# Optimization experiments

Hardware: AMD Instinct MI355X
Metric: run time of the kernel (lower is better)

Reference implementation:

```python
import jax, jax.numpy as jnp
import numpy as np

N_Q = 16
N_K = 16
D_QK = 64
D_V = 64
# torch module default scale=1.0 saturates softmax at feature width 1024;
# we use the conventional sqrt(d) scale for well-conditioned numerics.
SCALE = 32.0  # sqrt(N_Q * D_QK)
DROPOUT_P = 0.0  # dropout is identity at p=0


def setup_inputs() -> dict:
    key = jax.random.key(0)
    kq, kk, kv = jax.random.split(key, 3)
    S = 8192
    return {
        "query": jax.random.normal(kq, (S, N_Q, D_QK), dtype=jnp.float32),
        "key": jax.random.normal(kk, (S, N_K, D_QK), dtype=jnp.float32),
        "value": jax.random.normal(kv, (S, N_K, D_V), dtype=jnp.float32),
    }


def reference(query, key, value):
    # Flatten trailing (head, dim) into one feature axis, as the torch view does.
    q = query.reshape(-1, N_Q * D_QK)            # [S_q, 1024]
    k = key.reshape(-1, N_K * D_QK)              # [S_k, 1024]
    v = value.reshape(-1, N_K * D_V)             # [S_k, 1024]
    scores = jnp.matmul(q, k.T) / SCALE          # [S_q, S_k]
    attn = jax.nn.softmax(scores, axis=-1)       # dropout_p=0 -> identity
    out = jnp.matmul(attn, v)                    # [S_q, 1024]
    return out.reshape(query.shape[:-1] + (-1,))  # [S_q, N_Q, D_V]
```

## Files before the change

### kernel.cpp

```cpp
#include <hip/hip_runtime.h>
#include <hip/hip_bf16.h>


typedef __bf16 bf16x8 __attribute__((ext_vector_type(8)));
typedef float f32x4 __attribute__((ext_vector_type(4)));
typedef const __attribute__((address_space(1))) unsigned int* as1p;
typedef __attribute__((address_space(3))) unsigned int* as3p;
typedef unsigned short u16;

__device__ __forceinline__ u16 f2bf(float x) {
  unsigned u = __float_as_uint(x);
  u += 0x7fffu + ((u >> 16) & 1u);
  return (u16)(u >> 16);
}
__device__ __forceinline__ float bf2f(u16 b) { return __uint_as_float(((unsigned)b) << 16); }
__device__ __forceinline__ unsigned pack2(float lo, float hi) {
  return (unsigned)f2bf(lo) | ((unsigned)f2bf(hi) << 16);
}

#define BARX()   __builtin_amdgcn_s_barrier()
#define WAITL()  asm volatile("s_waitcnt lgkmcnt(0)")
#define WAITV(n) asm volatile("s_waitcnt vmcnt(" #n ")")

__global__ __launch_bounds__(256) void cvt_bf16(const float* __restrict__ in,
                                                unsigned short* __restrict__ out) {
  const size_t i = (size_t)blockIdx.x * 256 + threadIdx.x;
  const float4* p = (const float4*)in + i * 2;
  float4 a = p[0], b = p[1];
  uint4 o;
  o.x = pack2(a.x, a.y);
  o.y = pack2(a.z, a.w);
  o.z = pack2(b.x, b.y);
  o.w = pack2(b.z, b.w);
  ((uint4*)out)[i] = o;
}

__global__ __launch_bounds__(256) void transpose_bf16(const float* __restrict__ V,
                                                      unsigned short* __restrict__ VT) {
  __shared__ float t[64][65];
  const int rb = blockIdx.x * 64;
  const int cb = blockIdx.y * 64;
  const int tid = threadIdx.x;
#pragma unroll
  for (int it = 0; it < 4; ++it) {
    int r = it * 16 + (tid >> 4);
    int c = (tid & 15) * 4;
    float4 x = *(const float4*)(V + (size_t)(rb + r) * 1024 + cb + c);
    t[r][c] = x.x; t[r][c + 1] = x.y; t[r][c + 2] = x.z; t[r][c + 3] = x.w;
  }
  __syncthreads();
  const int j = tid & 63;
  const int c0 = (tid >> 6) * 16;
#pragma unroll
  for (int i = 0; i < 16; ++i) {
    int c = c0 + i;
    VT[(size_t)(cb + c) * 8192 + rb + j] = f2bf(t[j][c]);
  }
}

template <int BM, int OUTMODE, int DEC>
__global__ __launch_bounds__(512, 2) void gemm8d(const u16* __restrict__ A,
                                                 const u16* __restrict__ B,
                                                 void* __restrict__ Cv,
                                                 const float* __restrict__ inv,
                                                 float* __restrict__ partials,
                                                 int K, int ldc, float scale) {
  constexpr int MF = BM / 32;
  constexpr int MH = MF / 2;
  constexpr int ABUF = BM * 128;
  constexpr int BBUF = 32768;
  constexpr int BUFSZ = ABUF + BBUF;
  __shared__ __align__(1024) char smem[2 * BUFSZ];

  const int tid = threadIdx.x;
  const int lane = tid & 63, wave = tid >> 6;
  const int wr = wave >> 2, wc = wave & 3;
  const int lan15 = lane & 15, g = lane >> 4, l7 = lane & 7;

  const int nwg = gridDim.x;
  const int wg = (blockIdx.x & 7) * (nwg >> 3) + (blockIdx.x >> 3);
  int bm0, bn0;
  if constexpr (DEC == 0) {
    const int r = wg & 255;
    bm0 = (r >> 3) * 256;
    bn0 = (((wg >> 8) << 3) | (r & 7)) * 256;
  } else {
    const int chunk = wg >> 5;
    const int within = wg & 31;
    bm0 = (chunk * 8 + (within >> 2)) * BM;
    bn0 = (within & 3) * 256;
  }

  const int sr = tid >> 3;
  const int scb = ((tid & 7) ^ (sr & 7)) * 8;
  const u16* Ags = A + (size_t)(bm0 + sr) * K + scb;
  const u16* Bgs = B + (size_t)(bn0 + sr) * K + scb;

  const int sa0 = ((0 + g) ^ l7) * 16;
  const int sa1 = ((4 + g) ^ l7) * 16;
  const int abase = (wr * (BM / 2) + lan15) * 128;
  const int bbase = ABUF + (wc * 64 + lan15) * 128;

  f32x4 acc[MF][4];
#pragma unroll
  for (int m = 0; m < MF; ++m)
#pragma unroll
    for (int n = 0; n < 4; ++n) acc[m][n] = f32x4{0.f, 0.f, 0.f, 0.f};

  const int nt = K >> 6;
  const int niter = nt >> 1;

  auto IA = [&](int t, int ja, int jb) {
    char* bb = smem + (t & 1) * BUFSZ;
    const size_t ko = (size_t)t * 64;
    __builtin_amdgcn_global_load_lds((as1p)(Ags + (size_t)ja * 64 * K + ko),
                                     (as3p)(bb + ja * 8192 + tid * 16), 16, 0, 0);
    __builtin_amdgcn_global_load_lds((as1p)(Ags + (size_t)jb * 64 * K + ko),
                                     (as3p)(bb + jb * 8192 + tid * 16), 16, 0, 0);
  };
  auto IB = [&](int t, int j0) {
    char* bb = smem + (t & 1) * BUFSZ + ABUF;
    const size_t ko = (size_t)t * 64;
    __builtin_amdgcn_global_load_lds((as1p)(Bgs + (size_t)j0 * 64 * K + ko),
                                     (as3p)(bb + j0 * 8192 + tid * 16), 16, 0, 0);
    __builtin_amdgcn_global_load_lds((as1p)(Bgs + (size_t)(j0 + 1) * 64 * K + ko),
                                     (as3p)(bb + (j0 + 1) * 8192 + tid * 16), 16, 0, 0);
  };
  auto IA_mh0 = [&](int t) { if constexpr (BM == 256) IA(t, 0, 2); };
  auto IA_mh1 = [&](int t) { if constexpr (BM == 256) IA(t, 1, 3); else IA(t, 0, 1); };

  bf16x8 a[MH][2], b[4][2];
  auto DS_A = [&](int bb, int mh) {
#pragma unroll
    for (int m = 0; m < MH; ++m) {
      a[m][0] = *(const bf16x8*)(smem + bb + abase + (mh * MH + m) * 2048 + sa0);
      a[m][1] = *(const bf16x8*)(smem + bb + abase + (mh * MH + m) * 2048 + sa1);
    }
  };
  auto DS_B = [&](int bb, int nh) {
#pragma unroll
    for (int n = 0; n < 2; ++n) {
      b[nh * 2 + n][0] = *(const bf16x8*)(smem + bb + bbase + (nh * 2 + n) * 2048 + sa0);
      b[nh * 2 + n][1] = *(const bf16x8*)(smem + bb + bbase + (nh * 2 + n) * 2048 + sa1);
    }
  };
  auto MMA = [&](int mh, int nh) {
    __builtin_amdgcn_s_setprio(1);
#pragma unroll
    for (int m = 0; m < MH; ++m)
#pragma unroll
      for (int n = 0; n < 2; ++n)
#pragma unroll
        for (int ks = 0; ks < 2; ++ks)
          acc[mh * MH + m][nh * 2 + n] = __builtin_amdgcn_mfma_f32_16x16x32_bf16(
              a[m][ks], b[nh * 2 + n][ks], acc[mh * MH + m][nh * 2 + n], 0, 0, 0);
    __builtin_amdgcn_s_setprio(0);
  };

  if constexpr (BM == 256) {
    IA(0, 0, 2); IB(0, 0); IB(0, 2); IA(0, 1, 3);
    IA(1, 0, 2); IB(1, 0); IB(1, 2);
    WAITV(6);
  } else {
    IB(0, 0); IB(0, 2); IA(0, 0, 1);
    IB(1, 0); IB(1, 2);
    WAITV(4);
  }
  BARX();

  for (int i = 0; i < niter; ++i) {
    const int t0 = 2 * i;
    const bool more = (i + 1 < niter);

    DS_A(0, 0); DS_B(0, 0);
    IA_mh1(t0 + 1);
    BARX(); WAITL(); MMA(0, 0); BARX();

    DS_B(0, 1);
    if (more) IA_mh0(t0 + 2);
    BARX(); WAITL(); MMA(0, 1); BARX();

    DS_A(0, 1);
    if (more) IB(t0 + 2, 0);
    BARX(); WAITL(); MMA(1, 0); BARX();

    if (more) IB(t0 + 2, 2);
    BARX(); MMA(1, 1);
    if (more) { if constexpr (BM == 256) WAITV(6); else WAITV(4); } else { WAITV(0); }
    BARX();

    DS_A(BUFSZ, 0); DS_B(BUFSZ, 0);
    if (more) IA_mh1(t0 + 2);
    BARX(); WAITL(); MMA(0, 0); BARX();

    DS_B(BUFSZ, 1);
    if (more) IA_mh0(t0 + 3);
    BARX(); WAITL(); MMA(0, 1); BARX();

    DS_A(BUFSZ, 1);
    if (more) IB(t0 + 3, 0);
    BARX(); WAITL(); MMA(1, 0); BARX();

    if (more) IB(t0 + 3, 2);
    BARX(); MMA(1, 1);
    if (more) { if constexpr (BM == 256) WAITV(6); else WAITV(4); } else { WAITV(0); }
    BARX();
  }

  const int c0 = bn0 + wc * 64 + lan15;
  if constexpr (OUTMODE == 0) {
    u16* C = (u16*)Cv;
    const int cb4 = (bn0 >> 8) * 4 + wc;
#pragma unroll
    for (int m = 0; m < MF; ++m)
#pragma unroll
      for (int r = 0; r < 4; ++r) {
        const int row = bm0 + wr * (BM / 2) + m * 16 + g * 4 + r;
        float part = 0.f;
#pragma unroll
        for (int n = 0; n < 4; ++n) {
          float v = __expf(acc[m][n][r] * scale);
          C[(size_t)row * ldc + c0 + n * 16] = f2bf(v);
          part += v;
        }
        part += __shfl_xor(part, 1, 64);
        part += __shfl_xor(part, 2, 64);
        part += __shfl_xor(part, 4, 64);
        part += __shfl_xor(part, 8, 64);
        if (lan15 == 0) partials[(size_t)row * 128 + cb4] = part;
      }
  } else {
    float* C = (float*)Cv;
#pragma unroll
    for (int m = 0; m < MF; ++m)
#pragma unroll
      for (int r = 0; r < 4; ++r) {
        const int row = bm0 + wr * (BM / 2) + m * 16 + g * 4 + r;
        const float iv = inv ? inv[row] : 1.0f;
#pragma unroll
        for (int n = 0; n < 4; ++n)
          C[(size_t)row * ldc + c0 + n * 16] = acc[m][n][r] * iv;
      }
  }
}

__global__ __launch_bounds__(256) void rowinv(const float* __restrict__ partials,
                                              float* __restrict__ inv) {
  const int row = blockIdx.x * 256 + threadIdx.x;
  const float4* p = (const float4*)(partials + (size_t)row * 128);
  float s = 0.f;
#pragma unroll
  for (int j = 0; j < 32; ++j) {
    float4 v = p[j];
    s += (v.x + v.y) + (v.z + v.w);
  }
  inv[row] = 1.0f / s;
}

__global__ __launch_bounds__(256) void normalize_inplace(u16* __restrict__ E) {
  __shared__ float red[4];
  u16* row = E + (size_t)blockIdx.x * 8192;
  const int tid = threadIdx.x;
  float f[32];
  float s = 0.f;
#pragma unroll
  for (int c = 0; c < 4; ++c) {
    uint4 v = *((const uint4*)row + c * 256 + tid);
    unsigned u[4] = {v.x, v.y, v.z, v.w};
#pragma unroll
    for (int q = 0; q < 4; ++q) {
      f[c * 8 + q * 2] = bf2f((u16)(u[q] & 0xffffu));
      f[c * 8 + q * 2 + 1] = bf2f((u16)(u[q] >> 16));
      s += f[c * 8 + q * 2] + f[c * 8 + q * 2 + 1];
    }
  }
#pragma unroll
  for (int off = 32; off; off >>= 1) s += __shfl_xor(s, off, 64);
  if ((tid & 63) == 0) red[tid >> 6] = s;
  __syncthreads();
  const float iv = 1.0f / ((red[0] + red[1]) + (red[2] + red[3]));
#pragma unroll
  for (int c = 0; c < 4; ++c) {
    uint4 o;
    o.x = pack2(f[c * 8 + 0] * iv, f[c * 8 + 1] * iv);
    o.y = pack2(f[c * 8 + 2] * iv, f[c * 8 + 3] * iv);
    o.z = pack2(f[c * 8 + 4] * iv, f[c * 8 + 5] * iv);
    o.w = pack2(f[c * 8 + 6] * iv, f[c * 8 + 7] * iv);
    *((uint4*)row + c * 256 + tid) = o;
  }
}

extern "C" void kernel_launch(void* const* d_in, const int* in_sizes, int n_in,
                              void* d_out, int out_size, void* d_ws, size_t ws_size,
                              hipStream_t stream) {
  const float* Q = (const float*)d_in[0];
  const float* K = (const float*)d_in[1];
  const float* V = (const float*)d_in[2];

  char* ws = (char*)d_ws;
  u16* S = (u16*)ws;
  u16* VT = (u16*)(ws + (size_t)134217728);
  float* partials = (float*)(ws + (size_t)134217728 + 16777216);
  float* inv = (float*)(ws + (size_t)134217728 + 16777216 + 4194304);
  const bool haveInv =
      ws_size >= (size_t)134217728 + 16777216 + 4194304 + 32768;

  u16* Qb = (u16*)d_out;
  u16* Kb = Qb + 8388608;

  cvt_bf16<<<4096, 256, 0, stream>>>(Q, Qb);
  cvt_bf16<<<4096, 256, 0, stream>>>(K, Kb);
  transpose_bf16<<<dim3(128, 16), 256, 0, stream>>>(V, VT);

  gemm8d<256, 0, 0><<<1024, 512, 0, stream>>>(
      Qb, Kb, S, nullptr, haveInv ? partials : (float*)(ws + 134217728 + 16777216),
      1024, 8192, 1.0f / 32.0f);

  if (haveInv) {
    rowinv<<<32, 256, 0, stream>>>(partials, inv);
    gemm8d<128, 1, 1><<<256, 512, 0, stream>>>(
        S, VT, d_out, inv, nullptr, 8192, 1024, 1.0f);
  } else {
    normalize_inplace<<<8192, 256, 0, stream>>>(S);
    gemm8d<128, 1, 1><<<256, 512, 0, stream>>>(
        S, VT, d_out, nullptr, nullptr, 8192, 1024, 1.0f);
  }
}
```

Before: 303.0 us.

## Shrink GEMM tiles to 128x128 with four blocks per CU and simpler pipeline

Replaces the 256x256 and 128x256 GEMM tiles with a single 128x128 tile kernel sized for four resident workgroups per CU, with a simplified double-buffered load/MFMA schedule. The grids grow to 4096 and 512 blocks. Row-sum partials for the softmax are now reduced across the four column-waves in LDS before a single write per row, which halves the partials buffer and the rowinv reads. Smaller tiles are meant to raise occupancy and improve load balance. The cost is lower arithmetic intensity per tile and more global traffic for the operands.

After: 319.6 us. 5.5% more time.

```diff
diff --git a/kernel.cpp b/kernel.cpp
--- a/kernel.cpp
+++ b/kernel.cpp
@@ -58,18 +58,15 @@
   }
 }
 
-template <int BM, int OUTMODE, int DEC>
-__global__ __launch_bounds__(512, 2) void gemm8d(const u16* __restrict__ A,
+template <int OUTMODE, int DEC>
+__global__ __launch_bounds__(512, 4) void gemm2b(const u16* __restrict__ A,
                                                  const u16* __restrict__ B,
                                                  void* __restrict__ Cv,
                                                  const float* __restrict__ inv,
                                                  float* __restrict__ partials,
                                                  int K, int ldc, float scale) {
-  constexpr int MF = BM / 32;
-  constexpr int MH = MF / 2;
-  constexpr int ABUF = BM * 128;
-  constexpr int BBUF = 32768;
-  constexpr int BUFSZ = ABUF + BBUF;
+  constexpr int ABUF = 16384;
+  constexpr int BUFSZ = 32768;
   __shared__ __align__(1024) char smem[2 * BUFSZ];
 
   const int tid = threadIdx.x;
@@ -81,14 +78,16 @@
   const int wg = (blockIdx.x & 7) * (nwg >> 3) + (blockIdx.x >> 3);
   int bm0, bn0;
   if constexpr (DEC == 0) {
-    const int r = wg & 255;
-    bm0 = (r >> 3) * 256;
-    bn0 = (((wg >> 8) << 3) | (r & 7)) * 256;
+    const int chunk = wg >> 9;
+    const int r9 = wg & 511;
+    const int sub = r9 >> 6, win = r9 & 63;
+    bm0 = (chunk * 8 + (win >> 3)) * 128;
+    bn0 = (sub * 8 + (win & 7)) * 128;
   } else {
-    const int chunk = wg >> 5;
-    const int within = wg & 31;
-    bm0 = (chunk * 8 + (within >> 2)) * BM;
-    bn0 = (within & 3) * 256;
+    const int chunk = wg >> 6;
+    const int win = wg & 63;
+    bm0 = (chunk * 8 + (win >> 3)) * 128;
+    bn0 = (win & 7) * 128;
   }
 
   const int sr = tid >> 3;
@@ -98,127 +97,109 @@
 
   const int sa0 = ((0 + g) ^ l7) * 16;
   const int sa1 = ((4 + g) ^ l7) * 16;
-  const int abase = (wr * (BM / 2) + lan15) * 128;
-  const int bbase = ABUF + (wc * 64 + lan15) * 128;
-
-  f32x4 acc[MF][4];
-#pragma unroll
-  for (int m = 0; m < MF; ++m)
-#pragma unroll
-    for (int n = 0; n < 4; ++n) acc[m][n] = f32x4{0.f, 0.f, 0.f, 0.f};
+  const int abase = (wr * 64 + lan15) * 128;
+  const int bbase = ABUF + (wc * 32 + lan15) * 128;
+
+  f32x4 acc[4][2];
+#pragma unroll
+  for (int m = 0; m < 4; ++m)
+#pragma unroll
+    for (int n = 0; n < 2; ++n) acc[m][n] = f32x4{0.f, 0.f, 0.f, 0.f};
 
   const int nt = K >> 6;
   const int niter = nt >> 1;
 
-  auto IA = [&](int t, int ja, int jb) {
+  auto IA = [&](int t) {
     char* bb = smem + (t & 1) * BUFSZ;
     const size_t ko = (size_t)t * 64;
-    __builtin_amdgcn_global_load_lds((as1p)(Ags + (size_t)ja * 64 * K + ko),
-                                     (as3p)(bb + ja * 8192 + tid * 16), 16, 0, 0);
-    __builtin_amdgcn_global_load_lds((as1p)(Ags + (size_t)jb * 64 * K + ko),
-                                     (as3p)(bb + jb * 8192 + tid * 16), 16, 0, 0);
-  };
-  auto IB = [&](int t, int j0) {
+    __builtin_amdgcn_global_load_lds((as1p)(Ags + ko),
+                                     (as3p)(bb + tid * 16), 16, 0, 0);
+    __builtin_amdgcn_global_load_lds((as1p)(Ags + (size_t)64 * K + ko),
+                                     (as3p)(bb + 8192 + tid * 16), 16, 0, 0);
+  };
+  auto IB = [&](int t) {
     char* bb = smem + (t & 1) * BUFSZ + ABUF;
     const size_t ko = (size_t)t * 64;
-    __builtin_amdgcn_global_load_lds((as1p)(Bgs + (size_t)j0 * 64 * K + ko),
-                                     (as3p)(bb + j0 * 8192 + tid * 16), 16, 0, 0);
-    __builtin_amdgcn_global_load_lds((as1p)(Bgs + (size_t)(j0 + 1) * 64 * K + ko),
-                                     (as3p)(bb + (j0 + 1) * 8192 + tid * 16), 16, 0, 0);
-  };
-  auto IA_mh0 = [&](int t) { if constexpr (BM == 256) IA(t, 0, 2); };
-  auto IA_mh1 = [&](int t) { if constexpr (BM == 256) IA(t, 1, 3); else IA(t, 0, 1); };
-
-  bf16x8 a[MH][2], b[4][2];
+    __builtin_amdgcn_global_load_lds((as1p)(Bgs + ko),
+                                     (as3p)(bb + tid * 16), 16, 0, 0);
+    __builtin_amdgcn_global_load_lds((as1p)(Bgs + (size_t)64 * K + ko),
+                                     (as3p)(bb + 8192 + tid * 16), 16, 0, 0);
+  };
+
+  bf16x8 a[2][2], b[2][2];
   auto DS_A = [&](int bb, int mh) {
 #pragma unroll
-    for (int m = 0; m < MH; ++m) {
-      a[m][0] = *(const bf16x8*)(smem + bb + abase + (mh * MH + m) * 2048 + sa0);
-      a[m][1] = *(const bf16x8*)(smem + bb + abase + (mh * MH + m) * 2048 + sa1);
+    for (int m = 0; m < 2; ++m) {
+      a[m][0] = *(const bf16x8*)(smem + bb + abase + (mh * 2 + m) * 2048 + sa0);
+      a[m][1] = *(const bf16x8*)(smem + bb + abase + (mh * 2 + m) * 2048 + sa1);
     }
   };
-  auto DS_B = [&](int bb, int nh) {
+  auto DS_B = [&](int bb) {
 #pragma unroll
     for (int n = 0; n < 2; ++n) {
-      b[nh * 2 + n][0] = *(const bf16x8*)(smem + bb + bbase + (nh * 2 + n) * 2048 + sa0);
-      b[nh * 2 + n][1] = *(const bf16x8*)(smem + bb + bbase + (nh * 2 + n) * 2048 + sa1);
+      b[n][0] = *(const bf16x8*)(smem + bb + bbase + n * 2048 + sa0);
+      b[n][1] = *(const bf16x8*)(smem + bb + bbase + n * 2048 + sa1);
     }
   };
-  auto MMA = [&](int mh, int nh) {
+  auto MMA = [&](int mh) {
     __builtin_amdgcn_s_setprio(1);
 #pragma unroll
-    for (int m = 0; m < MH; ++m)
+    for (int m = 0; m < 2; ++m)
 #pragma unroll
       for (int n = 0; n < 2; ++n)
 #pragma unroll
         for (int ks = 0; ks < 2; ++ks)
-          acc[mh * MH + m][nh * 2 + n] = __builtin_amdgcn_mfma_f32_16x16x32_bf16(
-              a[m][ks], b[nh * 2 + n][ks], acc[mh * MH + m][nh * 2 + n], 0, 0, 0);
+          acc[mh * 2 + m][n] = __builtin_amdgcn_mfma_f32_16x16x32_bf16(
+              a[m][ks], b[n][ks], acc[mh * 2 + m][n], 0, 0, 0);
     __builtin_amdgcn_s_setprio(0);
   };
 
-  if constexpr (BM == 256) {
-    IA(0, 0, 2); IB(0, 0); IB(0, 2); IA(0, 1, 3);
-    IA(1, 0, 2); IB(1, 0); IB(1, 2);
-    WAITV(6);
-  } else {
-    IB(0, 0); IB(0, 2); IA(0, 0, 1);
-    IB(1, 0); IB(1, 2);
-    WAITV(4);
-  }
+  IA(0); IB(0); IA(1);
+  WAITV(2);
   BARX();
 
   for (int i = 0; i < niter; ++i) {
     const int t0 = 2 * i;
-    const bool more = (i + 1 < niter);
-
-    DS_A(0, 0); DS_B(0, 0);
-    IA_mh1(t0 + 1);
-    BARX(); WAITL(); MMA(0, 0); BARX();
-
-    DS_B(0, 1);
-    if (more) IA_mh0(t0 + 2);
-    BARX(); WAITL(); MMA(0, 1); BARX();
+    const bool more = (t0 + 2 < nt);
+
+    DS_A(0, 0); DS_B(0);
+    BARX(); WAITL();
+    IB(t0 + 1);
+    MMA(0);
+    BARX();
 
     DS_A(0, 1);
-    if (more) IB(t0 + 2, 0);
-    BARX(); WAITL(); MMA(1, 0); BARX();
-
-    if (more) IB(t0 + 2, 2);
-    BARX(); MMA(1, 1);
-    if (more) { if constexpr (BM == 256) WAITV(6); else WAITV(4); } else { WAITV(0); }
-    BARX();
-
-    DS_A(BUFSZ, 0); DS_B(BUFSZ, 0);
-    if (more) IA_mh1(t0 + 2);
-    BARX(); WAITL(); MMA(0, 0); BARX();
-
-    DS_B(BUFSZ, 1);
-    if (more) IA_mh0(t0 + 3);
-    BARX(); WAITL(); MMA(0, 1); BARX();
+    BARX(); WAITL();
+    if (more) { IA(t0 + 2); MMA(1); WAITV(2); }
+    else      { MMA(1); WAITV(0); }
+    BARX();
+
+    DS_A(BUFSZ, 0); DS_B(BUFSZ);
+    BARX(); WAITL();
+    if (more) IB(t0 + 2);
+    MMA(0);
+    BARX();
 
     DS_A(BUFSZ, 1);
-    if (more) IB(t0 + 3, 0);
-    BARX(); WAITL(); MMA(1, 0); BARX();
-
-    if (more) IB(t0 + 3, 2);
-    BARX(); MMA(1, 1);
-    if (more) { if constexpr (BM == 256) WAITV(6); else WAITV(4); } else { WAITV(0); }
-    BARX();
-  }
-
-  const int c0 = bn0 + wc * 64 + lan15;
+    BARX(); WAITL();
+    if (more) { IA(t0 + 3); MMA(1); WAITV(2); }
+    else      { MMA(1); }
+    BARX();
+  }
+
+  const int c0 = bn0 + wc * 32 + lan15;
   if constexpr (OUTMODE == 0) {
     u16* C = (u16*)Cv;
-    const int cb4 = (bn0 >> 8) * 4 + wc;
-#pragma unroll
-    for (int m = 0; m < MF; ++m)
+    float* red = (float*)smem;
+    float part_rows[4][4];
+#pragma unroll
+    for (int m = 0; m < 4; ++m)
 #pragma unroll
       for (int r = 0; r < 4; ++r) {
-        const int row = bm0 + wr * (BM / 2) + m * 16 + g * 4 + r;
+        const int row = bm0 + wr * 64 + m * 16 + g * 4 + r;
         float part = 0.f;
 #pragma unroll
-        for (int n = 0; n < 4; ++n) {
+        for (int n = 0; n < 2; ++n) {
           float v = __expf(acc[m][n][r] * scale);
           C[(size_t)row * ldc + c0 + n * 16] = f2bf(v);
           part += v;
@@ -227,18 +208,30 @@
         part += __shfl_xor(part, 2, 64);
         part += __shfl_xor(part, 4, 64);
         part += __shfl_xor(part, 8, 64);
-        if (lan15 == 0) partials[(size_t)row * 128 + cb4] = part;
+        part_rows[m][r] = part;
       }
+    BARX();
+#pragma unroll
+    for (int m = 0; m < 4; ++m)
+#pragma unroll
+      for (int r = 0; r < 4; ++r)
+        if (lan15 == 0)
+          red[(wr * 64 + m * 16 + g * 4 + r) * 4 + wc] = part_rows[m][r];
+    __syncthreads();
+    if (tid < 128) {
+      const float4 v = *(const float4*)&red[tid * 4];
+      partials[(size_t)(bm0 + tid) * 64 + (bn0 >> 7)] = (v.x + v.y) + (v.z + v.w);
+    }
   } else {
     float* C = (float*)Cv;
 #pragma unroll
-    for (int m = 0; m < MF; ++m)
+    for (int m = 0; m < 4; ++m)
 #pragma unroll
       for (int r = 0; r < 4; ++r) {
-        const int row = bm0 + wr * (BM / 2) + m * 16 + g * 4 + r;
+        const int row = bm0 + wr * 64 + m * 16 + g * 4 + r;
         const float iv = inv ? inv[row] : 1.0f;
 #pragma unroll
-        for (int n = 0; n < 4; ++n)
+        for (int n = 0; n < 2; ++n)
           C[(size_t)row * ldc + c0 + n * 16] = acc[m][n][r] * iv;
       }
   }
@@ -247,10 +240,10 @@
 __global__ __launch_bounds__(256) void rowinv(const float* __restrict__ partials,
                                               float* __restrict__ inv) {
   const int row = blockIdx.x * 256 + threadIdx.x;
-  const float4* p = (const float4*)(partials + (size_t)row * 128);
+  const float4* p = (const float4*)(partials + (size_t)row * 64);
   float s = 0.f;
 #pragma unroll
-  for (int j = 0; j < 32; ++j) {
+  for (int j = 0; j < 16; ++j) {
     float4 v = p[j];
     s += (v.x + v.y) + (v.z + v.w);
   }
@@ -312,17 +305,17 @@
   cvt_bf16<<<4096, 256, 0, stream>>>(K, Kb);
   transpose_bf16<<<dim3(128, 16), 256, 0, stream>>>(V, VT);
 
-  gemm8d<256, 0, 0><<<1024, 512, 0, stream>>>(
+  gemm2b<0, 0><<<4096, 512, 0, stream>>>(
       Qb, Kb, S, nullptr, haveInv ? partials : (float*)(ws + 134217728 + 16777216),
       1024, 8192, 1.0f / 32.0f);
 
   if (haveInv) {
     rowinv<<<32, 256, 0, stream>>>(partials, inv);
-    gemm8d<128, 1, 1><<<256, 512, 0, stream>>>(
+    gemm2b<1, 1><<<512, 512, 0, stream>>>(
         S, VT, d_out, inv, nullptr, 8192, 1024, 1.0f);
   } else {
     normalize_inplace<<<8192, 256, 0, stream>>>(S);
-    gemm8d<128, 1, 1><<<256, 512, 0, stream>>>(
+    gemm2b<1, 1><<<512, 512, 0, stream>>>(
         S, VT, d_out, nullptr, nullptr, 8192, 1024, 1.0f);
   }
 }
```

## Switch GEMM tiles from 16x16x32 to 32x32x16 bf16 MFMA

Applied to the files above, without the earlier changes.

Replaces the 16x16x32 MFMA fragments with 32x32x16 MFMA. Each wave now holds 32x32 accumulator blocks, and the LDS fragment loads are reorganized into four k-slices with matching swizzle offsets. The epilogue row mapping and the row-sum shuffle reduction are updated for the 32-lane layout. The intent is to cut LDS read traffic per FLOP and raise MFMA throughput per instruction. The cost is a different register and LDS access pattern, which could cause bank conflicts or register pressure.

After: 362.6 us. 1.2x slower.

```diff
diff --git a/kernel.cpp b/kernel.cpp
--- a/kernel.cpp
+++ b/kernel.cpp
@@ -3,7 +3,7 @@
 
 
 typedef __bf16 bf16x8 __attribute__((ext_vector_type(8)));
-typedef float f32x4 __attribute__((ext_vector_type(4)));
+typedef float f32x16 __attribute__((ext_vector_type(16)));
 typedef const __attribute__((address_space(1))) unsigned int* as1p;
 typedef __attribute__((address_space(3))) unsigned int* as3p;
 typedef unsigned short u16;
@@ -59,14 +59,14 @@
 }
 
 template <int BM, int OUTMODE, int DEC>
-__global__ __launch_bounds__(512, 2) void gemm8d(const u16* __restrict__ A,
+__global__ __launch_bounds__(512, 2) void gemm32(const u16* __restrict__ A,
                                                  const u16* __restrict__ B,
                                                  void* __restrict__ Cv,
                                                  const float* __restrict__ inv,
                                                  float* __restrict__ partials,
                                                  int K, int ldc, float scale) {
-  constexpr int MF = BM / 32;
-  constexpr int MH = MF / 2;
+  constexpr int NRB = BM / 64;
+  constexpr int MHT = NRB / 2;
   constexpr int ABUF = BM * 128;
   constexpr int BBUF = 32768;
   constexpr int BUFSZ = ABUF + BBUF;
@@ -75,7 +75,7 @@
   const int tid = threadIdx.x;
   const int lane = tid & 63, wave = tid >> 6;
   const int wr = wave >> 2, wc = wave & 3;
-  const int lan15 = lane & 15, g = lane >> 4, l7 = lane & 7;
+  const int l31 = lane & 31, lg = lane >> 5, l7 = lane & 7;
 
   const int nwg = gridDim.x;
   const int wg = (blockIdx.x & 7) * (nwg >> 3) + (blockIdx.x >> 3);
@@ -96,16 +96,19 @@
   const u16* Ags = A + (size_t)(bm0 + sr) * K + scb;
   const u16* Bgs = B + (size_t)(bn0 + sr) * K + scb;
 
-  const int sa0 = ((0 + g) ^ l7) * 16;
-  const int sa1 = ((4 + g) ^ l7) * 16;
-  const int abase = (wr * (BM / 2) + lan15) * 128;
-  const int bbase = ABUF + (wc * 64 + lan15) * 128;
-
-  f32x4 acc[MF][4];
-#pragma unroll
-  for (int m = 0; m < MF; ++m)
-#pragma unroll
-    for (int n = 0; n < 4; ++n) acc[m][n] = f32x4{0.f, 0.f, 0.f, 0.f};
+  int sk[4];
+#pragma unroll
+  for (int ks = 0; ks < 4; ++ks) sk[ks] = ((ks * 2 + lg) ^ l7) * 16;
+  const int abase = (wr * (BM / 2) + l31) * 128;
+  const int bbase = ABUF + (wc * 64 + l31) * 128;
+
+  f32x16 acc[NRB][2];
+#pragma unroll
+  for (int m = 0; m < NRB; ++m)
+#pragma unroll
+    for (int n = 0; n < 2; ++n)
+#pragma unroll
+      for (int r = 0; r < 16; ++r) acc[m][n][r] = 0.f;
 
   const int nt = K >> 6;
   const int niter = nt >> 1;
@@ -129,31 +132,27 @@
   auto IA_mh0 = [&](int t) { if constexpr (BM == 256) IA(t, 0, 2); };
   auto IA_mh1 = [&](int t) { if constexpr (BM == 256) IA(t, 1, 3); else IA(t, 0, 1); };
 
-  bf16x8 a[MH][2], b[4][2];
+  bf16x8 a[MHT][4], b[2][4];
   auto DS_A = [&](int bb, int mh) {
 #pragma unroll
-    for (int m = 0; m < MH; ++m) {
-      a[m][0] = *(const bf16x8*)(smem + bb + abase + (mh * MH + m) * 2048 + sa0);
-      a[m][1] = *(const bf16x8*)(smem + bb + abase + (mh * MH + m) * 2048 + sa1);
-    }
+    for (int t = 0; t < MHT; ++t)
+#pragma unroll
+      for (int ks = 0; ks < 4; ++ks)
+        a[t][ks] = *(const bf16x8*)(smem + bb + abase + (mh * MHT + t) * 4096 + sk[ks]);
   };
   auto DS_B = [&](int bb, int nh) {
 #pragma unroll
-    for (int n = 0; n < 2; ++n) {
-      b[nh * 2 + n][0] = *(const bf16x8*)(smem + bb + bbase + (nh * 2 + n) * 2048 + sa0);
-      b[nh * 2 + n][1] = *(const bf16x8*)(smem + bb + bbase + (nh * 2 + n) * 2048 + sa1);
-    }
+    for (int ks = 0; ks < 4; ++ks)
+      b[nh][ks] = *(const bf16x8*)(smem + bb + bbase + nh * 4096 + sk[ks]);
   };
   auto MMA = [&](int mh, int nh) {
     __builtin_amdgcn_s_setprio(1);
 #pragma unroll
-    for (int m = 0; m < MH; ++m)
-#pragma unroll
-      for (int n = 0; n < 2; ++n)
-#pragma unroll
-        for (int ks = 0; ks < 2; ++ks)
-          acc[mh * MH + m][nh * 2 + n] = __builtin_amdgcn_mfma_f32_16x16x32_bf16(
-              a[m][ks], b[nh * 2 + n][ks], acc[mh * MH + m][nh * 2 + n], 0, 0, 0);
+    for (int t = 0; t < MHT; ++t)
+#pragma unroll
+      for (int ks = 0; ks < 4; ++ks)
+        acc[mh * MHT + t][nh] = __builtin_amdgcn_mfma_f32_32x32x16_bf16(
+            a[t][ks], b[nh][ks], acc[mh * MHT + t][nh], 0, 0, 0);
     __builtin_amdgcn_s_setprio(0);
   };
 
@@ -207,39 +206,39 @@
     BARX();
   }
 
-  const int c0 = bn0 + wc * 64 + lan15;
+  const int c0 = bn0 + wc * 64 + l31;
   if constexpr (OUTMODE == 0) {
     u16* C = (u16*)Cv;
     const int cb4 = (bn0 >> 8) * 4 + wc;
 #pragma unroll
-    for (int m = 0; m < MF; ++m)
-#pragma unroll
-      for (int r = 0; r < 4; ++r) {
-        const int row = bm0 + wr * (BM / 2) + m * 16 + g * 4 + r;
-        float part = 0.f;
-#pragma unroll
-        for (int n = 0; n < 4; ++n) {
-          float v = __expf(acc[m][n][r] * scale);
-          C[(size_t)row * ldc + c0 + n * 16] = f2bf(v);
-          part += v;
-        }
+    for (int rb = 0; rb < NRB; ++rb)
+#pragma unroll
+      for (int reg = 0; reg < 16; ++reg) {
+        const int row = bm0 + wr * (BM / 2) + rb * 32 +
+                        (reg & 3) + 8 * (reg >> 2) + 4 * lg;
+        const float v0 = __expf(acc[rb][0][reg] * scale);
+        const float v1 = __expf(acc[rb][1][reg] * scale);
+        C[(size_t)row * ldc + c0] = f2bf(v0);
+        C[(size_t)row * ldc + c0 + 32] = f2bf(v1);
+        float part = v0 + v1;
         part += __shfl_xor(part, 1, 64);
         part += __shfl_xor(part, 2, 64);
         part += __shfl_xor(part, 4, 64);
         part += __shfl_xor(part, 8, 64);
-        if (lan15 == 0) partials[(size_t)row * 128 + cb4] = part;
+        part += __shfl_xor(part, 16, 64);
+        if (l31 == 0) partials[(size_t)row * 128 + cb4] = part;
       }
   } else {
     float* C = (float*)Cv;
 #pragma unroll
-    for (int m = 0; m < MF; ++m)
-#pragma unroll
-      for (int r = 0; r < 4; ++r) {
-        const int row = bm0 + wr * (BM / 2) + m * 16 + g * 4 + r;
+    for (int rb = 0; rb < NRB; ++rb)
+#pragma unroll
+      for (int reg = 0; reg < 16; ++reg) {
+        const int row = bm0 + wr * (BM / 2) + rb * 32 +
+                        (reg & 3) + 8 * (reg >> 2) + 4 * lg;
         const float iv = inv ? inv[row] : 1.0f;
-#pragma unroll
-        for (int n = 0; n < 4; ++n)
-          C[(size_t)row * ldc + c0 + n * 16] = acc[m][n][r] * iv;
+        C[(size_t)row * ldc + c0] = acc[rb][0][reg] * iv;
+        C[(size_t)row * ldc + c0 + 32] = acc[rb][1][reg] * iv;
       }
   }
 }
@@ -312,17 +311,17 @@
   cvt_bf16<<<4096, 256, 0, stream>>>(K, Kb);
   transpose_bf16<<<dim3(128, 16), 256, 0, stream>>>(V, VT);
 
-  gemm8d<256, 0, 0><<<1024, 512, 0, stream>>>(
+  gemm32<256, 0, 0><<<1024, 512, 0, stream>>>(
       Qb, Kb, S, nullptr, haveInv ? partials : (float*)(ws + 134217728 + 16777216),
       1024, 8192, 1.0f / 32.0f);
 
   if (haveInv) {
     rowinv<<<32, 256, 0, stream>>>(partials, inv);
-    gemm8d<128, 1, 1><<<256, 512, 0, stream>>>(
+    gemm32<128, 1, 1><<<256, 512, 0, stream>>>(
         S, VT, d_out, inv, nullptr, 8192, 1024, 1.0f);
   } else {
     normalize_inplace<<<8192, 256, 0, stream>>>(S);
-    gemm8d<128, 1, 1><<<256, 512, 0, stream>>>(
+    gemm32<128, 1, 1><<<256, 512, 0, stream>>>(
         S, VT, d_out, nullptr, nullptr, 8192, 1024, 1.0f);
   }
 }
```
